# Optimization experiments

Hardware: AMD Instinct MI355X
Metric: run time of the kernel (lower is better)

Reference implementation:

```python
import jax, jax.numpy as jnp
import numpy as np

N, H, E, T = 100000, 128, 500000, 6  # nodes, hidden, max edges, edge types


def setup_inputs() -> dict:
    key = jax.random.key(0)
    ks = jax.random.split(key, 16)
    xav_e = float(np.sqrt(6.0 / (H + T * H)))  # xavier_uniform for edge_dense
    xav_h = float(np.sqrt(6.0 / (H + H)))
    u = lambda k, s, a: jax.random.uniform(k, s, jnp.float32, -a, a)
    return {
        "node_embeddings": jax.random.normal(ks[0], (N, H), jnp.float32),
        "W_edge": u(ks[1], (H, T * H), xav_e),
        "b_edge": 1e-6 * jax.random.normal(ks[2], (T * H,), jnp.float32),
        "W_ir": u(ks[3], (H, H), xav_h), "b_ir": jnp.zeros((H,), jnp.float32),
        "W_iz": u(ks[4], (H, H), xav_h), "b_iz": jnp.zeros((H,), jnp.float32),
        "W_in": u(ks[5], (H, H), xav_h), "b_in": jnp.zeros((H,), jnp.float32),
        "W_hr": u(ks[6], (H, H), xav_h),
        "W_hz": u(ks[7], (H, H), xav_h),
        "W_hn": u(ks[8], (H, H), xav_h), "b_hn": jnp.zeros((H,), jnp.float32),
        "source_indices": jax.random.randint(ks[9], (E,), 0, N, jnp.int32),
        "dest_indices": jax.random.randint(ks[10], (E,), 0, N, jnp.int32),
        "edge_types": jax.random.randint(ks[11], (E,), 0, T, jnp.int32),
        "num_edges": 450000,
    }


def reference(node_embeddings, W_edge, b_edge, W_ir, b_ir, W_iz, b_iz,
              W_in, b_in, W_hr, W_hz, W_hn, b_hn,
              source_indices, dest_indices, edge_types, num_edges):
    num_nodes, hidden = node_embeddings.shape
    max_edges = edge_types.shape[0]
    # gather source nodes, project to all edge types at once: [E, T*H]
    src = node_embeddings[source_indices]
    all_types = (src @ W_edge + b_edge).reshape(max_edges, -1, hidden)  # [E,T,H]
    # select per-edge type
    msg = jnp.take_along_axis(all_types, edge_types[:, None, None], axis=1)[:, 0, :]
    # mask padding edges, scatter-add into destination nodes
    msg = jnp.where((jnp.arange(max_edges) < num_edges)[:, None], msg, 0)
    agg = jax.ops.segment_sum(msg, dest_indices, num_segments=num_nodes)
    # GRU update: carry h = aggregated messages, inputs x = node_embeddings
    h, x = agg, node_embeddings
    r = jax.nn.sigmoid(x @ W_ir + b_ir + h @ W_hr)
    z = jax.nn.sigmoid(x @ W_iz + b_iz + h @ W_hz)
    n = jnp.tanh(x @ W_in + b_in + r * (h @ W_hn + b_hn))
    return (1.0 - z) * n + z * h
```

## Files before the change

kernel.cpp:

```cpp
#include <hip/hip_runtime.h>
#include <hip/hip_bf16.h>

#define HD 128
#define NT 6

typedef unsigned short u16;
typedef unsigned int u32;
typedef __attribute__((ext_vector_type(8))) short bf16x8;
typedef __attribute__((ext_vector_type(4))) float f32x4;

__device__ __forceinline__ float sigmoidf_(float x) {
  return 1.0f / (1.0f + __expf(-x));
}

__device__ __forceinline__ u16 f2bf(float x) {
  u32 u = __float_as_uint(x);
  return (u16)((u + 0x7FFFu + ((u >> 16) & 1u)) >> 16);
}
__device__ __forceinline__ float bflo(u32 v) { return __uint_as_float(v << 16); }
__device__ __forceinline__ float bfhi(u32 v) { return __uint_as_float(v & 0xffff0000u); }
__device__ __forceinline__ float bfs(u16 v) { return __uint_as_float((u32)v << 16); }

__device__ __forceinline__ int swz(int p) { return p ^ (((p >> 8) & 7) << 4); }

__global__ void k_cvt_w(const float* __restrict__ We,
                        const float* __restrict__ Wir, const float* __restrict__ Wiz,
                        const float* __restrict__ Win, const float* __restrict__ Whr,
                        const float* __restrict__ Whz, const float* __restrict__ Whn,
                        u16* __restrict__ WeT, u16* __restrict__ WgT) {
  int i = blockIdx.x * blockDim.x + threadIdx.x;
  if (i < NT * HD * HD) {
    int c = i >> 7, k = i & 127;
    WeT[i] = f2bf(We[(size_t)k * (NT * HD) + c]);
  } else {
    int j = i - NT * HD * HD;
    if (j < 6 * HD * HD) {
      int m = j >> 14, jj = j & 16383;
      int c = jj >> 7, k = jj & 127;
      const float* W = (m == 0) ? Wir : (m == 1) ? Wiz : (m == 2) ? Win
                     : (m == 3) ? Whr : (m == 4) ? Whz : Whn;
      WgT[j] = f2bf(W[(size_t)k * HD + c]);
    }
  }
}

__global__ __launch_bounds__(256) void k_gemm_edge6(
    const float* __restrict__ X, const u16* __restrict__ WeT,
    const float* __restrict__ Be, u16* __restrict__ P, int N)
{
  __shared__ char As[32768];
  __shared__ char Bs[32768];
  const int tid = threadIdx.x;
  const int row0 = blockIdx.x * 128;

  #pragma unroll
  for (int i = 0; i < 8; ++i) {
    int p = i * 4096 + tid * 16;
    int row = row0 + (p >> 8);
    union { u16 u[8]; bf16x8 v; } ra;
    if (row < N) {
      const float4* s = (const float4*)(X + (size_t)row0 * HD + (p >> 1));
      float4 f0 = s[0], f1 = s[1];
      ra.u[0] = f2bf(f0.x); ra.u[1] = f2bf(f0.y); ra.u[2] = f2bf(f0.z); ra.u[3] = f2bf(f0.w);
      ra.u[4] = f2bf(f1.x); ra.u[5] = f2bf(f1.y); ra.u[6] = f2bf(f1.z); ra.u[7] = f2bf(f1.w);
    } else {
      #pragma unroll
      for (int j = 0; j < 8; ++j) ra.u[j] = 0;
    }
    *(bf16x8*)(As + swz(p)) = ra.v;
  }

  const int l = tid & 63, w = tid >> 6;
  const int m0 = (w >> 1) * 64, n0 = (w & 1) * 64;
  const int lr = l & 15, lg = l >> 4;
  f32x4 zero = {0.f, 0.f, 0.f, 0.f};

  for (int t = 0; t < NT; ++t) {
    __syncthreads();
    const char* gB = (const char*)(WeT + (size_t)t * HD * HD);
    #pragma unroll
    for (int i = 0; i < 8; ++i) {
      int p = i * 4096 + tid * 16;
      *(bf16x8*)(Bs + swz(p)) = *(const bf16x8*)(gB + p);
    }
    __syncthreads();

    f32x4 acc[4][4];
    #pragma unroll
    for (int m = 0; m < 4; ++m)
      #pragma unroll
      for (int n = 0; n < 4; ++n) acc[m][n] = zero;

    #pragma unroll
    for (int k = 0; k < 4; ++k) {
      bf16x8 a[4], b[4];
      #pragma unroll
      for (int m = 0; m < 4; ++m)
        a[m] = *(const bf16x8*)(As + swz((m0 + m * 16 + lr) * 256 + k * 64 + lg * 16));
      #pragma unroll
      for (int n = 0; n < 4; ++n)
        b[n] = *(const bf16x8*)(Bs + swz((n0 + n * 16 + lr) * 256 + k * 64 + lg * 16));
      #pragma unroll
      for (int m = 0; m < 4; ++m)
        #pragma unroll
        for (int n = 0; n < 4; ++n)
          acc[m][n] = __builtin_amdgcn_mfma_f32_16x16x32_bf16(a[m], b[n], acc[m][n], 0, 0, 0);
    }

    float bias[4];
    #pragma unroll
    for (int n = 0; n < 4; ++n) bias[n] = Be[t * HD + n0 + n * 16 + lr];
    #pragma unroll
    for (int m = 0; m < 4; ++m) {
      int rbase = row0 + m0 + m * 16 + lg * 4;
      #pragma unroll
      for (int j = 0; j < 4; ++j) {
        int row = rbase + j;
        if (row < N) {
          #pragma unroll
          for (int n = 0; n < 4; ++n)
            P[(size_t)row * (NT * HD) + t * HD + n0 + n * 16 + lr] =
                f2bf(acc[m][n][j] + bias[n]);
        }
      }
    }
  }
}

__global__ __launch_bounds__(256) void k_count(const int* __restrict__ dst,
                                               const int* __restrict__ nePtr,
                                               int* __restrict__ deg) {
  const int ne = nePtr[0];
  for (int e = blockIdx.x * blockDim.x + threadIdx.x; e < ne;
       e += gridDim.x * blockDim.x)
    atomicAdd(&deg[dst[e]], 1);
}

__global__ __launch_bounds__(256) void k_scan_a(const int* __restrict__ deg,
                                                int* __restrict__ off,
                                                int* __restrict__ bsum, int N) {
  __shared__ int s[256];
  const int b = blockIdx.x, tid = threadIdx.x;
  const int base = b * 1024 + tid * 4;
  int v0 = 0, v1 = 0, v2 = 0, v3 = 0;
  if (base < N) v0 = deg[base];
  if (base + 1 < N) v1 = deg[base + 1];
  if (base + 2 < N) v2 = deg[base + 2];
  if (base + 3 < N) v3 = deg[base + 3];
  const int sum = v0 + v1 + v2 + v3;
  s[tid] = sum;
  __syncthreads();
  for (int d = 1; d < 256; d <<= 1) {
    int t = (tid >= d) ? s[tid - d] : 0;
    __syncthreads();
    s[tid] += t;
    __syncthreads();
  }
  const int excl = s[tid] - sum;
  if (base < N) off[base] = excl;
  if (base + 1 < N) off[base + 1] = excl + v0;
  if (base + 2 < N) off[base + 2] = excl + v0 + v1;
  if (base + 3 < N) off[base + 3] = excl + v0 + v1 + v2;
  if (tid == 255) bsum[b] = s[255];
}

__global__ void k_scan_b(int* __restrict__ bsum, int nb) {
  __shared__ int s[1024];
  const int tid = threadIdx.x;
  const int v = (tid < nb) ? bsum[tid] : 0;
  s[tid] = v;
  __syncthreads();
  for (int d = 1; d < 1024; d <<= 1) {
    int t = (tid >= d) ? s[tid - d] : 0;
    __syncthreads();
    s[tid] += t;
    __syncthreads();
  }
  if (tid < nb) bsum[tid] = s[tid] - v;
}

__global__ __launch_bounds__(256) void k_scan_c(int* __restrict__ off,
                                                const int* __restrict__ bsum, int N) {
  const int b = blockIdx.x, tid = threadIdx.x;
  const int add = bsum[b];
  const int base = b * 1024 + tid * 4;
  #pragma unroll
  for (int i = 0; i < 4; ++i)
    if (base + i < N) off[base + i] += add;
}

__global__ __launch_bounds__(256) void k_fill(const int* __restrict__ src,
                                              const int* __restrict__ dst,
                                              const int* __restrict__ typ,
                                              const int* __restrict__ nePtr,
                                              int* __restrict__ off,
                                              u32* __restrict__ elist) {
  const int ne = nePtr[0];
  for (int e = blockIdx.x * blockDim.x + threadIdx.x; e < ne;
       e += gridDim.x * blockDim.x) {
    int pos = atomicAdd(&off[dst[e]], 1);
    elist[pos] = (u32)(src[e] * NT + typ[e]);
  }
}

__global__ __launch_bounds__(256) void k_gather(
    const u16* __restrict__ P, const int* __restrict__ deg,
    const int* __restrict__ off, const u32* __restrict__ elist,
    u16* __restrict__ Hb, int N)
{
  const int l = threadIdx.x & 63;
  int wid = (int)((blockIdx.x * blockDim.x + threadIdx.x) >> 6);
  int nw = (int)((gridDim.x * blockDim.x) >> 6);
  for (int n = wid; n < N; n += nw) {
    const int e1 = off[n];
    const int e0 = e1 - deg[n];
    float a0 = 0.f, a1 = 0.f, b0 = 0.f, b1 = 0.f;
    for (int e = e0; e < e1; e += 4) {
      u32 p0 = elist[e];
      u32 p1 = (e + 1 < e1) ? elist[e + 1] : p0;
      u32 p2 = (e + 2 < e1) ? elist[e + 2] : p0;
      u32 p3 = (e + 3 < e1) ? elist[e + 3] : p0;
      u32 v0 = *((const u32*)(P + (size_t)p0 * HD) + l);
      u32 v1 = *((const u32*)(P + (size_t)p1 * HD) + l);
      u32 v2 = *((const u32*)(P + (size_t)p2 * HD) + l);
      u32 v3 = *((const u32*)(P + (size_t)p3 * HD) + l);
      if (e + 1 >= e1) v1 = 0;
      if (e + 2 >= e1) v2 = 0;
      if (e + 3 >= e1) v3 = 0;
      a0 += bflo(v0); a1 += bfhi(v0);
      b0 += bflo(v1); b1 += bfhi(v1);
      a0 += bflo(v2); a1 += bfhi(v2);
      b0 += bflo(v3); b1 += bfhi(v3);
    }
    a0 += b0; a1 += b1;
    u32 hp = ((u32)f2bf(a1) << 16) | (u32)f2bf(a0);
    *((u32*)(Hb + (size_t)n * HD) + l) = hp;
  }
}

__global__ __launch_bounds__(512) void k_gru15(
    const float* __restrict__ X, const u16* __restrict__ Hb,
    const u16* __restrict__ WgT,
    const float* __restrict__ bir, const float* __restrict__ biz,
    const float* __restrict__ bin_, const float* __restrict__ bhn,
    float* __restrict__ out, int N)
{
  __shared__ char Xs[32768];
  __shared__ char Hs[32768];
  __shared__ char Bs[2][32768];
  const int tid = threadIdx.x;
  const int row0 = blockIdx.x * 128;

  #pragma unroll
  for (int i = 0; i < 4; ++i) {
    int p = i * 8192 + tid * 16;
    int row = row0 + (p >> 8);
    union { u16 u[8]; bf16x8 v; } rx, rh;
    if (row < N) {
      const float4* sx = (const float4*)(X + (size_t)row0 * HD + (p >> 1));
      float4 x0 = sx[0], x1 = sx[1];
      rx.u[0] = f2bf(x0.x); rx.u[1] = f2bf(x0.y); rx.u[2] = f2bf(x0.z); rx.u[3] = f2bf(x0.w);
      rx.u[4] = f2bf(x1.x); rx.u[5] = f2bf(x1.y); rx.u[6] = f2bf(x1.z); rx.u[7] = f2bf(x1.w);
      rh.v = *(const bf16x8*)((const char*)Hb + (size_t)row0 * 256 + p);
    } else {
      #pragma unroll
      for (int j = 0; j < 8; ++j) { rx.u[j] = 0; rh.u[j] = 0; }
    }
    *(bf16x8*)(Xs + swz(p)) = rx.v;
    *(bf16x8*)(Hs + swz(p)) = rh.v;
  }

  const int l = tid & 63, w = tid >> 6;
  const int m0 = (w >> 1) * 32;
  const int n0 = (w & 1) * 64;
  const int lr = l & 15, lg = l >> 4;
  f32x4 zero = {0.f, 0.f, 0.f, 0.f};

  bf16x8 wreg[4];
  auto loadW = [&](int g) {
    const char* gp = (const char*)(WgT + (size_t)g * HD * HD);
    #pragma unroll
    for (int i = 0; i < 4; ++i)
      wreg[i] = *(const bf16x8*)(gp + i * 8192 + tid * 16);
  };
  auto writeW = [&](int buf) {
    #pragma unroll
    for (int i = 0; i < 4; ++i) {
      int p = i * 8192 + tid * 16;
      *(bf16x8*)(Bs[buf] + swz(p)) = wreg[i];
    }
  };

  auto sweep = [&](const char* Ab, int buf, f32x4 (&acc)[2][4]) {
    #pragma unroll
    for (int m = 0; m < 2; ++m)
      #pragma unroll
      for (int n = 0; n < 4; ++n) acc[m][n] = zero;
    #pragma unroll
    for (int k = 0; k < 4; ++k) {
      bf16x8 a[2], b[4];
      #pragma unroll
      for (int m = 0; m < 2; ++m)
        a[m] = *(const bf16x8*)(Ab + swz((m0 + m * 16 + lr) * 256 + k * 64 + lg * 16));
      #pragma unroll
      for (int n = 0; n < 4; ++n)
        b[n] = *(const bf16x8*)(Bs[buf] + swz((n0 + n * 16 + lr) * 256 + k * 64 + lg * 16));
      #pragma unroll
      for (int m = 0; m < 2; ++m)
        #pragma unroll
        for (int n = 0; n < 4; ++n)
          acc[m][n] = __builtin_amdgcn_mfma_f32_16x16x32_bf16(a[m], b[n], acc[m][n], 0, 0, 0);
    }
  };

  f32x4 t1[2][4], t2[2][4], rg[2][4], nn[2][4];
  float bv[4];
  auto ldBias = [&](const float* bp) {
    #pragma unroll
    for (int n = 0; n < 4; ++n) bv[n] = bp[n0 + n * 16 + lr];
  };

  loadW(0); writeW(0);
  __syncthreads();

  loadW(3);
  sweep(Xs, 0, t1);
  writeW(1);
  __syncthreads();

  loadW(5);
  sweep(Hs, 1, t2);
  writeW(0);
  ldBias(bir);
  #pragma unroll
  for (int m = 0; m < 2; ++m)
    #pragma unroll
    for (int n = 0; n < 4; ++n)
      #pragma unroll
      for (int j = 0; j < 4; ++j)
        rg[m][n][j] = sigmoidf_(t1[m][n][j] + bv[n] + t2[m][n][j]);
  __syncthreads();

  loadW(2);
  sweep(Hs, 0, t2);
  writeW(1);
  ldBias(bhn);
  #pragma unroll
  for (int m = 0; m < 2; ++m)
    #pragma unroll
    for (int n = 0; n < 4; ++n)
      #pragma unroll
      for (int j = 0; j < 4; ++j)
        rg[m][n][j] *= (t2[m][n][j] + bv[n]);
  __syncthreads();

  loadW(1);
  sweep(Xs, 1, t1);
  writeW(0);
  ldBias(bin_);
  #pragma unroll
  for (int m = 0; m < 2; ++m)
    #pragma unroll
    for (int n = 0; n < 4; ++n)
      #pragma unroll
      for (int j = 0; j < 4; ++j)
        nn[m][n][j] = tanhf(t1[m][n][j] + bv[n] + rg[m][n][j]);
  __syncthreads();

  loadW(4);
  sweep(Xs, 0, t1);
  writeW(1);
  __syncthreads();

  sweep(Hs, 1, t2);
  ldBias(biz);
  #pragma unroll
  for (int m = 0; m < 2; ++m) {
    #pragma unroll
    for (int j = 0; j < 4; ++j) {
      int row = row0 + m0 + m * 16 + lg * 4 + j;
      if (row < N) {
        #pragma unroll
        for (int n = 0; n < 4; ++n) {
          int col = n0 + n * 16 + lr;
          float z = sigmoidf_(t1[m][n][j] + bv[n] + t2[m][n][j]);
          float h = bfs(Hb[(size_t)row * HD + col]);
          out[(size_t)row * HD + col] = (1.0f - z) * nn[m][n][j] + z * h;
        }
      }
    }
  }
}

__global__ __launch_bounds__(256) void k_gather_gru(
    const float* __restrict__ X, const u16* __restrict__ P,
    const int* __restrict__ deg, const int* __restrict__ off,
    const u32* __restrict__ elist, const u16* __restrict__ WgT,
    const float* __restrict__ bir, const float* __restrict__ biz,
    const float* __restrict__ bin_, const float* __restrict__ bhn,
    float* __restrict__ out, int N)
{
  __shared__ char Xs[16384];
  __shared__ char Hs[16384];
  const int tid = threadIdx.x;
  const int l = tid & 63, w = tid >> 6;
  const int row0 = blockIdx.x * 64;
  const int wr0 = w * 16;

  #pragma unroll
  for (int it = 0; it < 4; ++it) {
    int chunk = it * 64 + l;
    int r = chunk >> 4, seg = chunk & 15;
    int grow = row0 + wr0 + r;
    union { u16 u[8]; bf16x8 v; } rx;
    if (grow < N) {
      const float4* sx = (const float4*)(X + (size_t)grow * HD + seg * 8);
      float4 x0 = sx[0], x1 = sx[1];
      rx.u[0] = f2bf(x0.x); rx.u[1] = f2bf(x0.y); rx.u[2] = f2bf(x0.z); rx.u[3] = f2bf(x0.w);
      rx.u[4] = f2bf(x1.x); rx.u[5] = f2bf(x1.y); rx.u[6] = f2bf(x1.z); rx.u[7] = f2bf(x1.w);
    } else {
      #pragma unroll
      for (int j = 0; j < 8; ++j) rx.u[j] = 0;
    }
    *(bf16x8*)(Xs + swz((wr0 + r) * 256 + seg * 16)) = rx.v;
  }

  for (int i = 0; i < 16; ++i) {
    int n = row0 + wr0 + i;
    float a0 = 0.f, a1 = 0.f;
    if (n < N) {
      int e1 = off[n];
      for (int e = e1 - deg[n]; e < e1; e += 4) {
        u32 p0 = elist[e];
        u32 p1 = (e + 1 < e1) ? elist[e + 1] : p0;
        u32 p2 = (e + 2 < e1) ? elist[e + 2] : p0;
        u32 p3 = (e + 3 < e1) ? elist[e + 3] : p0;
        u32 v0 = *((const u32*)(P + (size_t)p0 * HD) + l);
        u32 v1 = *((const u32*)(P + (size_t)p1 * HD) + l);
        u32 v2 = *((const u32*)(P + (size_t)p2 * HD) + l);
        u32 v3 = *((const u32*)(P + (size_t)p3 * HD) + l);
        if (e + 1 >= e1) v1 = 0;
        if (e + 2 >= e1) v2 = 0;
        if (e + 3 >= e1) v3 = 0;
        a0 += bflo(v0) + bflo(v1) + bflo(v2) + bflo(v3);
        a1 += bfhi(v0) + bfhi(v1) + bfhi(v2) + bfhi(v3);
      }
    }
    u32 hp = ((u32)f2bf(a1) << 16) | (u32)f2bf(a0);
    *(u32*)(Hs + swz((wr0 + i) * 256 + l * 4)) = hp;
  }

  const int lr = l & 15, lg = l >> 4;
  const int rloc = wr0;

  f32x4 zero = {0.f, 0.f, 0.f, 0.f};
  auto sweep = [&](const char* Ab, const u16* WT, f32x4* acc) {
    #pragma unroll
    for (int n = 0; n < 8; ++n) acc[n] = zero;
    #pragma unroll
    for (int k = 0; k < 4; ++k) {
      bf16x8 a = *(const bf16x8*)(Ab + swz((rloc + lr) * 256 + k * 64 + lg * 16));
      #pragma unroll
      for (int n = 0; n < 8; ++n) {
        bf16x8 b = *(const bf16x8*)(WT + (size_t)(n * 16 + lr) * HD + k * 32 + lg * 8);
        acc[n] = __builtin_amdgcn_mfma_f32_16x16x32_bf16(a, b, acc[n], 0, 0, 0);
      }
    }
  };

  f32x4 t1[8], t2[8], rg[8], nn[8];
  float bv[8];

  sweep(Xs, WgT + 0 * HD * HD, t1);
  sweep(Hs, WgT + 3 * HD * HD, t2);
  #pragma unroll
  for (int n = 0; n < 8; ++n) bv[n] = bir[n * 16 + lr];
  #pragma unroll
  for (int n = 0; n < 8; ++n)
    #pragma unroll
    for (int j = 0; j < 4; ++j) rg[n][j] = sigmoidf_(t1[n][j] + bv[n] + t2[n][j]);

  sweep(Hs, WgT + 5 * HD * HD, t2);
  #pragma unroll
  for (int n = 0; n < 8; ++n) bv[n] = bhn[n * 16 + lr];
  #pragma unroll
  for (int n = 0; n < 8; ++n)
    #pragma unroll
    for (int j = 0; j < 4; ++j) rg[n][j] *= (t2[n][j] + bv[n]);

  sweep(Xs, WgT + 2 * HD * HD, t1);
  #pragma unroll
  for (int n = 0; n < 8; ++n) bv[n] = bin_[n * 16 + lr];
  #pragma unroll
  for (int n = 0; n < 8; ++n)
    #pragma unroll
    for (int j = 0; j < 4; ++j) nn[n][j] = tanhf(t1[n][j] + bv[n] + rg[n][j]);

  sweep(Xs, WgT + 1 * HD * HD, t1);
  sweep(Hs, WgT + 4 * HD * HD, t2);
  #pragma unroll
  for (int n = 0; n < 8; ++n) bv[n] = biz[n * 16 + lr];
  #pragma unroll
  for (int n = 0; n < 8; ++n) {
    #pragma unroll
    for (int j = 0; j < 4; ++j) {
      int row = row0 + rloc + lg * 4 + j;
      if (row < N) {
        float z = sigmoidf_(t1[n][j] + bv[n] + t2[n][j]);
        u16 hu = *(const u16*)(Hs + swz((rloc + lg * 4 + j) * 256 + (n * 16 + lr) * 2));
        out[(size_t)row * HD + n * 16 + lr] = (1.0f - z) * nn[n][j] + z * bfs(hu);
      }
    }
  }
}

__global__ __launch_bounds__(256) void k_scatter(
    const u16* __restrict__ P, const int* __restrict__ src,
    const int* __restrict__ dst, const int* __restrict__ typ,
    const int* __restrict__ nePtr, float* __restrict__ agg,
    int ldP, int fixedType)
{
  const int ne = nePtr[0];
  const int lane = threadIdx.x & 63;
  const int wid = (int)((blockIdx.x * blockDim.x + threadIdx.x) >> 6);
  const int nw = (int)((gridDim.x * blockDim.x) >> 6);
  for (int e = wid; e < ne; e += nw) {
    const int t = typ[e];
    if (fixedType >= 0 && t != fixedType) continue;
    const size_t po = (ldP == HD) ? (size_t)src[e] * HD
                                  : (size_t)src[e] * (NT * HD) + (size_t)t * HD;
    u32 v = *(const u32*)(P + po + lane * 2);
    float* o = agg + (size_t)dst[e] * HD + lane * 2;
    unsafeAtomicAdd(o, bflo(v));
    unsafeAtomicAdd(o + 1, bfhi(v));
  }
}

__global__ __launch_bounds__(256) void k_gru(
    const float* __restrict__ X, const float* __restrict__ agg,
    const u16* __restrict__ WgT,
    const float* __restrict__ bir, const float* __restrict__ biz,
    const float* __restrict__ bin_, const float* __restrict__ bhn,
    float* __restrict__ out, int N)
{
  __shared__ char Xs[16384];
  __shared__ char Hs[16384];
  const int tid = threadIdx.x;
  const int row0 = blockIdx.x * 64;

  #pragma unroll
  for (int i = 0; i < 4; ++i) {
    int p = i * 4096 + tid * 16;
    int row = row0 + (p >> 8);
    union { u16 u[8]; bf16x8 v; } rx, rh;
    if (row < N) {
      const float4* sx = (const float4*)(X + (size_t)row0 * HD + (p >> 1));
      const float4* sh = (const float4*)(agg + (size_t)row0 * HD + (p >> 1));
      float4 x0 = sx[0], x1 = sx[1], h0 = sh[0], h1 = sh[1];
      rx.u[0] = f2bf(x0.x); rx.u[1] = f2bf(x0.y); rx.u[2] = f2bf(x0.z); rx.u[3] = f2bf(x0.w);
      rx.u[4] = f2bf(x1.x); rx.u[5] = f2bf(x1.y); rx.u[6] = f2bf(x1.z); rx.u[7] = f2bf(x1.w);
      rh.u[0] = f2bf(h0.x); rh.u[1] = f2bf(h0.y); rh.u[2] = f2bf(h0.z); rh.u[3] = f2bf(h0.w);
      rh.u[4] = f2bf(h1.x); rh.u[5] = f2bf(h1.y); rh.u[6] = f2bf(h1.z); rh.u[7] = f2bf(h1.w);
    } else {
      #pragma unroll
      for (int j = 0; j < 8; ++j) { rx.u[j] = 0; rh.u[j] = 0; }
    }
    *(bf16x8*)(Xs + swz(p)) = rx.v;
    *(bf16x8*)(Hs + swz(p)) = rh.v;
  }
  __syncthreads();

  const int l = tid & 63, w = tid >> 6;
  const int lr = l & 15, lg = l >> 4;
  const int rloc = w * 16;

  f32x4 zero = {0.f, 0.f, 0.f, 0.f};
  auto sweep = [&](const char* Ab, const u16* WT, f32x4* acc) {
    #pragma unroll
    for (int n = 0; n < 8; ++n) acc[n] = zero;
    #pragma unroll
    for (int k = 0; k < 4; ++k) {
      bf16x8 a = *(const bf16x8*)(Ab + swz((rloc + lr) * 256 + k * 64 + lg * 16));
      #pragma unroll
      for (int n = 0; n < 8; ++n) {
        bf16x8 b = *(const bf16x8*)(WT + (size_t)(n * 16 + lr) * HD + k * 32 + lg * 8);
        acc[n] = __builtin_amdgcn_mfma_f32_16x16x32_bf16(a, b, acc[n], 0, 0, 0);
      }
    }
  };

  f32x4 t1[8], t2[8], rg[8], nn[8];
  float bv[8];

  sweep(Xs, WgT + 0 * HD * HD, t1);
  sweep(Hs, WgT + 3 * HD * HD, t2);
  #pragma unroll
  for (int n = 0; n < 8; ++n) bv[n] = bir[n * 16 + lr];
  #pragma unroll
  for (int n = 0; n < 8; ++n)
    #pragma unroll
    for (int j = 0; j < 4; ++j) rg[n][j] = sigmoidf_(t1[n][j] + bv[n] + t2[n][j]);

  sweep(Hs, WgT + 5 * HD * HD, t2);
  #pragma unroll
  for (int n = 0; n < 8; ++n) bv[n] = bhn[n * 16 + lr];
  #pragma unroll
  for (int n = 0; n < 8; ++n)
    #pragma unroll
    for (int j = 0; j < 4; ++j) rg[n][j] *= (t2[n][j] + bv[n]);

  sweep(Xs, WgT + 2 * HD * HD, t1);
  #pragma unroll
  for (int n = 0; n < 8; ++n) bv[n] = bin_[n * 16 + lr];
  #pragma unroll
  for (int n = 0; n < 8; ++n)
    #pragma unroll
    for (int j = 0; j < 4; ++j) nn[n][j] = tanhf(t1[n][j] + bv[n] + rg[n][j]);

  sweep(Xs, WgT + 1 * HD * HD, t1);
  sweep(Hs, WgT + 4 * HD * HD, t2);
  #pragma unroll
  for (int n = 0; n < 8; ++n) bv[n] = biz[n * 16 + lr];
  #pragma unroll
  for (int n = 0; n < 8; ++n) {
    #pragma unroll
    for (int j = 0; j < 4; ++j) {
      int row = row0 + rloc + lg * 4 + j;
      if (row < N) {
        float z = sigmoidf_(t1[n][j] + bv[n] + t2[n][j]);
        float h = agg[(size_t)row * HD + n * 16 + lr];
        out[(size_t)row * HD + n * 16 + lr] = (1.0f - z) * nn[n][j] + z * h;
      }
    }
  }
}

extern "C" void kernel_launch(void* const* d_in, const int* in_sizes, int n_in,
                              void* d_out, int out_size, void* d_ws, size_t ws_size,
                              hipStream_t stream) {
  const float* X      = (const float*)d_in[0];
  const float* W_edge = (const float*)d_in[1];
  const float* b_edge = (const float*)d_in[2];
  const float* b_ir   = (const float*)d_in[4];
  const float* b_iz   = (const float*)d_in[6];
  const float* b_in   = (const float*)d_in[8];
  const float* b_hn   = (const float*)d_in[12];
  const int* src      = (const int*)d_in[13];
  const int* dst      = (const int*)d_in[14];
  const int* typ      = (const int*)d_in[15];
  const int* nePtr    = (const int*)d_in[16];

  const int N = in_sizes[0] / HD;
  const int E = in_sizes[13];
  char* ws = (char*)d_ws;

  size_t cur = 0;
  auto alloc = [&](size_t bytes) {
    size_t p = cur;
    cur = (cur + bytes + 255) & ~(size_t)255;
    return p;
  };
  u16* WeT   = (u16*)(ws + alloc((size_t)NT * HD * HD * 2));
  u16* WgT   = (u16*)(ws + alloc((size_t)6 * HD * HD * 2));
  int* deg   = (int*)(ws + alloc((size_t)N * 4));
  int* offA  = (int*)(ws + alloc((size_t)N * 4));
  int* bsum  = (int*)(ws + alloc(1024 * 4));
  u32* elist = (u32*)(ws + alloc((size_t)E * 4));
  size_t base_need = cur;
  u16* P     = (u16*)(ws + alloc((size_t)N * NT * HD * 2));
  const size_t csr_need = cur;
  u16* Hb    = (u16*)(ws + alloc((size_t)N * HD * 2));
  const size_t split_need = cur;

  const int gb = (N + 127) / 128;
  const int NB = (N + 1023) / 1024;

  k_cvt_w<<<(NT * HD * HD + 6 * HD * HD + 255) / 256, 256, 0, stream>>>(
      W_edge, (const float*)d_in[3], (const float*)d_in[5], (const float*)d_in[7],
      (const float*)d_in[9], (const float*)d_in[10], (const float*)d_in[11], WeT, WgT);

  if (ws_size >= csr_need) {
    hipMemsetAsync(deg, 0, (size_t)N * 4, stream);
    k_gemm_edge6<<<gb, 256, 0, stream>>>(X, WeT, b_edge, P, N);
    k_count<<<1024, 256, 0, stream>>>(dst, nePtr, deg);
    k_scan_a<<<NB, 256, 0, stream>>>(deg, offA, bsum, N);
    k_scan_b<<<1, 1024, 0, stream>>>(bsum, NB);
    k_scan_c<<<NB, 256, 0, stream>>>(offA, bsum, N);
    k_fill<<<1024, 256, 0, stream>>>(src, dst, typ, nePtr, offA, elist);
    if (ws_size >= split_need) {
      k_gather<<<(N + 3) / 4, 256, 0, stream>>>(P, deg, offA, elist, Hb, N);
      k_gru15<<<gb, 512, 0, stream>>>(
          X, Hb, WgT, b_ir, b_iz, b_in, b_hn, (float*)d_out, N);
    } else {
      k_gather_gru<<<(N + 63) / 64, 256, 0, stream>>>(
          X, P, deg, offA, elist, WgT, b_ir, b_iz, b_in, b_hn, (float*)d_out, N);
    }
  } else {
    float* agg = (float*)d_out;
    hipMemsetAsync(d_out, 0, (size_t)out_size * sizeof(float), stream);
    size_t pneed = base_need + (size_t)N * NT * HD * 2;
    if (ws_size >= pneed) {
      u16* Pf = (u16*)(ws + base_need);
      k_gemm_edge6<<<gb, 256, 0, stream>>>(X, WeT, b_edge, Pf, N);
      k_scatter<<<2048, 256, 0, stream>>>(Pf, src, dst, typ, nePtr, agg, NT * HD, -1);
      k_gru<<<(N + 63) / 64, 256, 0, stream>>>(X, agg, WgT, b_ir, b_iz, b_in, b_hn, agg, N);
    }
  }
}
```

Baseline: 236.6 us.

## Fuse CSR gather into LDS-staged GRU kernel, drop separate gather pass

Replaces the separate gather kernel and split GRU kernel with one fused kernel. Each 512-thread block gathers the aggregated messages for its 128 rows straight into shared memory, then runs the double-buffered LDS weight GEMM pipeline. The bf16 Hb intermediate no longer makes a global round trip and one launch goes away. The cost is that the irregular gather now shares occupancy with a 128KB-LDS block, so gather latency hiding may suffer.

```diff
diff --git a/kernel.cpp b/kernel.cpp
--- a/kernel.cpp
+++ b/kernel.cpp
@@ -203,44 +203,10 @@
   }
 }
 
-__global__ __launch_bounds__(256) void k_gather(
-    const u16* __restrict__ P, const int* __restrict__ deg,
-    const int* __restrict__ off, const u32* __restrict__ elist,
-    u16* __restrict__ Hb, int N)
-{
-  const int l = threadIdx.x & 63;
-  int wid = (int)((blockIdx.x * blockDim.x + threadIdx.x) >> 6);
-  int nw = (int)((gridDim.x * blockDim.x) >> 6);
-  for (int n = wid; n < N; n += nw) {
-    const int e1 = off[n];
-    const int e0 = e1 - deg[n];
-    float a0 = 0.f, a1 = 0.f, b0 = 0.f, b1 = 0.f;
-    for (int e = e0; e < e1; e += 4) {
-      u32 p0 = elist[e];
-      u32 p1 = (e + 1 < e1) ? elist[e + 1] : p0;
-      u32 p2 = (e + 2 < e1) ? elist[e + 2] : p0;
-      u32 p3 = (e + 3 < e1) ? elist[e + 3] : p0;
-      u32 v0 = *((const u32*)(P + (size_t)p0 * HD) + l);
-      u32 v1 = *((const u32*)(P + (size_t)p1 * HD) + l);
-      u32 v2 = *((const u32*)(P + (size_t)p2 * HD) + l);
-      u32 v3 = *((const u32*)(P + (size_t)p3 * HD) + l);
-      if (e + 1 >= e1) v1 = 0;
-      if (e + 2 >= e1) v2 = 0;
-      if (e + 3 >= e1) v3 = 0;
-      a0 += bflo(v0); a1 += bfhi(v0);
-      b0 += bflo(v1); b1 += bfhi(v1);
-      a0 += bflo(v2); a1 += bfhi(v2);
-      b0 += bflo(v3); b1 += bfhi(v3);
-    }
-    a0 += b0; a1 += b1;
-    u32 hp = ((u32)f2bf(a1) << 16) | (u32)f2bf(a0);
-    *((u32*)(Hb + (size_t)n * HD) + l) = hp;
-  }
-}
-
-__global__ __launch_bounds__(512) void k_gru15(
-    const float* __restrict__ X, const u16* __restrict__ Hb,
-    const u16* __restrict__ WgT,
+__global__ __launch_bounds__(512) void k_gru16(
+    const float* __restrict__ X, const u16* __restrict__ P,
+    const int* __restrict__ deg, const int* __restrict__ off,
+    const u32* __restrict__ elist, const u16* __restrict__ WgT,
     const float* __restrict__ bir, const float* __restrict__ biz,
     const float* __restrict__ bin_, const float* __restrict__ bhn,
     float* __restrict__ out, int N)
@@ -249,32 +215,9 @@
   __shared__ char Hs[32768];
   __shared__ char Bs[2][32768];
   const int tid = threadIdx.x;
+  const int l = tid & 63, w = tid >> 6;
   const int row0 = blockIdx.x * 128;
-
-  #pragma unroll
-  for (int i = 0; i < 4; ++i) {
-    int p = i * 8192 + tid * 16;
-    int row = row0 + (p >> 8);
-    union { u16 u[8]; bf16x8 v; } rx, rh;
-    if (row < N) {
-      const float4* sx = (const float4*)(X + (size_t)row0 * HD + (p >> 1));
-      float4 x0 = sx[0], x1 = sx[1];
-      rx.u[0] = f2bf(x0.x); rx.u[1] = f2bf(x0.y); rx.u[2] = f2bf(x0.z); rx.u[3] = f2bf(x0.w);
-      rx.u[4] = f2bf(x1.x); rx.u[5] = f2bf(x1.y); rx.u[6] = f2bf(x1.z); rx.u[7] = f2bf(x1.w);
-      rh.v = *(const bf16x8*)((const char*)Hb + (size_t)row0 * 256 + p);
-    } else {
-      #pragma unroll
-      for (int j = 0; j < 8; ++j) { rx.u[j] = 0; rh.u[j] = 0; }
-    }
-    *(bf16x8*)(Xs + swz(p)) = rx.v;
-    *(bf16x8*)(Hs + swz(p)) = rh.v;
-  }
-
-  const int l = tid & 63, w = tid >> 6;
-  const int m0 = (w >> 1) * 32;
-  const int n0 = (w & 1) * 64;
-  const int lr = l & 15, lg = l >> 4;
-  f32x4 zero = {0.f, 0.f, 0.f, 0.f};
+  const int wr0 = w * 16;
 
   bf16x8 wreg[4];
   auto loadW = [&](int g) {
@@ -291,121 +234,7 @@
     }
   };
 
-  auto sweep = [&](const char* Ab, int buf, f32x4 (&acc)[2][4]) {
-    #pragma unroll
-    for (int m = 0; m < 2; ++m)
-      #pragma unroll
-      for (int n = 0; n < 4; ++n) acc[m][n] = zero;
-    #pragma unroll
-    for (int k = 0; k < 4; ++k) {
-      bf16x8 a[2], b[4];
-      #pragma unroll
-      for (int m = 0; m < 2; ++m)
-        a[m] = *(const bf16x8*)(Ab + swz((m0 + m * 16 + lr) * 256 + k * 64 + lg * 16));
-      #pragma unroll
-      for (int n = 0; n < 4; ++n)
-        b[n] = *(const bf16x8*)(Bs[buf] + swz((n0 + n * 16 + lr) * 256 + k * 64 + lg * 16));
-      #pragma unroll
-      for (int m = 0; m < 2; ++m)
-        #pragma unroll
-        for (int n = 0; n < 4; ++n)
-          acc[m][n] = __builtin_amdgcn_mfma_f32_16x16x32_bf16(a[m], b[n], acc[m][n], 0, 0, 0);
-    }
-  };
-
-  f32x4 t1[2][4], t2[2][4], rg[2][4], nn[2][4];
-  float bv[4];
-  auto ldBias = [&](const float* bp) {
-    #pragma unroll
-    for (int n = 0; n < 4; ++n) bv[n] = bp[n0 + n * 16 + lr];
-  };
-
-  loadW(0); writeW(0);
-  __syncthreads();
-
-  loadW(3);
-  sweep(Xs, 0, t1);
-  writeW(1);
-  __syncthreads();
-
-  loadW(5);
-  sweep(Hs, 1, t2);
-  writeW(0);
-  ldBias(bir);
-  #pragma unroll
-  for (int m = 0; m < 2; ++m)
-    #pragma unroll
-    for (int n = 0; n < 4; ++n)
-      #pragma unroll
-      for (int j = 0; j < 4; ++j)
-        rg[m][n][j] = sigmoidf_(t1[m][n][j] + bv[n] + t2[m][n][j]);
-  __syncthreads();
-
-  loadW(2);
-  sweep(Hs, 0, t2);
-  writeW(1);
-  ldBias(bhn);
-  #pragma unroll
-  for (int m = 0; m < 2; ++m)
-    #pragma unroll
-    for (int n = 0; n < 4; ++n)
-      #pragma unroll
-      for (int j = 0; j < 4; ++j)
-        rg[m][n][j] *= (t2[m][n][j] + bv[n]);
-  __syncthreads();
-
-  loadW(1);
-  sweep(Xs, 1, t1);
-  writeW(0);
-  ldBias(bin_);
-  #pragma unroll
-  for (int m = 0; m < 2; ++m)
-    #pragma unroll
-    for (int n = 0; n < 4; ++n)
-      #pragma unroll
-      for (int j = 0; j < 4; ++j)
-        nn[m][n][j] = tanhf(t1[m][n][j] + bv[n] + rg[m][n][j]);
-  __syncthreads();
-
-  loadW(4);
-  sweep(Xs, 0, t1);
-  writeW(1);
-  __syncthreads();
-
-  sweep(Hs, 1, t2);
-  ldBias(biz);
-  #pragma unroll
-  for (int m = 0; m < 2; ++m) {
-    #pragma unroll
-    for (int j = 0; j < 4; ++j) {
-      int row = row0 + m0 + m * 16 + lg * 4 + j;
-      if (row < N) {
-        #pragma unroll
-        for (int n = 0; n < 4; ++n) {
-          int col = n0 + n * 16 + lr;
-          float z = sigmoidf_(t1[m][n][j] + bv[n] + t2[m][n][j]);
-          float h = bfs(Hb[(size_t)row * HD + col]);
-          out[(size_t)row * HD + col] = (1.0f - z) * nn[m][n][j] + z * h;
-        }
-      }
-    }
-  }
-}
-
-__global__ __launch_bounds__(256) void k_gather_gru(
-    const float* __restrict__ X, const u16* __restrict__ P,
-    const int* __restrict__ deg, const int* __restrict__ off,
-    const u32* __restrict__ elist, const u16* __restrict__ WgT,
-    const float* __restrict__ bir, const float* __restrict__ biz,
-    const float* __restrict__ bin_, const float* __restrict__ bhn,
-    float* __restrict__ out, int N)
-{
-  __shared__ char Xs[16384];
-  __shared__ char Hs[16384];
-  const int tid = threadIdx.x;
-  const int l = tid & 63, w = tid >> 6;
-  const int row0 = blockIdx.x * 64;
-  const int wr0 = w * 16;
+  loadW(0);
 
   #pragma unroll
   for (int it = 0; it < 4; ++it) {
@@ -427,7 +256,7 @@
 
   for (int i = 0; i < 16; ++i) {
     int n = row0 + wr0 + i;
-    float a0 = 0.f, a1 = 0.f;
+    float a0 = 0.f, a1 = 0.f, b0 = 0.f, b1 = 0.f;
     if (n < N) {
       int e1 = off[n];
       for (int e = e1 - deg[n]; e < e1; e += 4) {
@@ -442,73 +271,119 @@
         if (e + 1 >= e1) v1 = 0;
         if (e + 2 >= e1) v2 = 0;
         if (e + 3 >= e1) v3 = 0;
-        a0 += bflo(v0) + bflo(v1) + bflo(v2) + bflo(v3);
-        a1 += bfhi(v0) + bfhi(v1) + bfhi(v2) + bfhi(v3);
+        a0 += bflo(v0); a1 += bfhi(v0);
+        b0 += bflo(v1); b1 += bfhi(v1);
+        a0 += bflo(v2); a1 += bfhi(v2);
+        b0 += bflo(v3); b1 += bfhi(v3);
       }
     }
+    a0 += b0; a1 += b1;
     u32 hp = ((u32)f2bf(a1) << 16) | (u32)f2bf(a0);
     *(u32*)(Hs + swz((wr0 + i) * 256 + l * 4)) = hp;
   }
 
+  const int m0 = (w >> 1) * 32;
+  const int n0 = (w & 1) * 64;
   const int lr = l & 15, lg = l >> 4;
-  const int rloc = wr0;
-
   f32x4 zero = {0.f, 0.f, 0.f, 0.f};
-  auto sweep = [&](const char* Ab, const u16* WT, f32x4* acc) {
-    #pragma unroll
-    for (int n = 0; n < 8; ++n) acc[n] = zero;
+
+  auto sweep = [&](const char* Ab, int buf, f32x4 (&acc)[2][4]) {
+    #pragma unroll
+    for (int m = 0; m < 2; ++m)
+      #pragma unroll
+      for (int n = 0; n < 4; ++n) acc[m][n] = zero;
     #pragma unroll
     for (int k = 0; k < 4; ++k) {
-      bf16x8 a = *(const bf16x8*)(Ab + swz((rloc + lr) * 256 + k * 64 + lg * 16));
-      #pragma unroll
-      for (int n = 0; n < 8; ++n) {
-        bf16x8 b = *(const bf16x8*)(WT + (size_t)(n * 16 + lr) * HD + k * 32 + lg * 8);
-        acc[n] = __builtin_amdgcn_mfma_f32_16x16x32_bf16(a, b, acc[n], 0, 0, 0);
-      }
+      bf16x8 a[2], b[4];
+      #pragma unroll
+      for (int m = 0; m < 2; ++m)
+        a[m] = *(const bf16x8*)(Ab + swz((m0 + m * 16 + lr) * 256 + k * 64 + lg * 16));
+      #pragma unroll
+      for (int n = 0; n < 4; ++n)
+        b[n] = *(const bf16x8*)(Bs[buf] + swz((n0 + n * 16 + lr) * 256 + k * 64 + lg * 16));
+      #pragma unroll
+      for (int m = 0; m < 2; ++m)
+        #pragma unroll
+        for (int n = 0; n < 4; ++n)
+          acc[m][n] = __builtin_amdgcn_mfma_f32_16x16x32_bf16(a[m], b[n], acc[m][n], 0, 0, 0);
     }
   };
 
-  f32x4 t1[8], t2[8], rg[8], nn[8];
-  float bv[8];
-
-  sweep(Xs, WgT + 0 * HD * HD, t1);
-  sweep(Hs, WgT + 3 * HD * HD, t2);
-  #pragma unroll
-  for (int n = 0; n < 8; ++n) bv[n] = bir[n * 16 + lr];
-  #pragma unroll
-  for (int n = 0; n < 8; ++n)
-    #pragma unroll
-    for (int j = 0; j < 4; ++j) rg[n][j] = sigmoidf_(t1[n][j] + bv[n] + t2[n][j]);
-
-  sweep(Hs, WgT + 5 * HD * HD, t2);
-  #pragma unroll
-  for (int n = 0; n < 8; ++n) bv[n] = bhn[n * 16 + lr];
-  #pragma unroll
-  for (int n = 0; n < 8; ++n)
-    #pragma unroll
-    for (int j = 0; j < 4; ++j) rg[n][j] *= (t2[n][j] + bv[n]);
-
-  sweep(Xs, WgT + 2 * HD * HD, t1);
-  #pragma unroll
-  for (int n = 0; n < 8; ++n) bv[n] = bin_[n * 16 + lr];
-  #pragma unroll
-  for (int n = 0; n < 8; ++n)
-    #pragma unroll
-    for (int j = 0; j < 4; ++j) nn[n][j] = tanhf(t1[n][j] + bv[n] + rg[n][j]);
-
-  sweep(Xs, WgT + 1 * HD * HD, t1);
-  sweep(Hs, WgT + 4 * HD * HD, t2);
-  #pragma unroll
-  for (int n = 0; n < 8; ++n) bv[n] = biz[n * 16 + lr];
-  #pragma unroll
-  for (int n = 0; n < 8; ++n) {
+  f32x4 t1[2][4], t2[2][4], rg[2][4], nn[2][4];
+  float bv[4];
+  auto ldBias = [&](const float* bp) {
+    #pragma unroll
+    for (int n = 0; n < 4; ++n) bv[n] = bp[n0 + n * 16 + lr];
+  };
+
+  writeW(0);
+  __syncthreads();
+
+  loadW(3);
+  sweep(Xs, 0, t1);
+  writeW(1);
+  __syncthreads();
+
+  loadW(5);
+  sweep(Hs, 1, t2);
+  writeW(0);
+  ldBias(bir);
+  #pragma unroll
+  for (int m = 0; m < 2; ++m)
+    #pragma unroll
+    for (int n = 0; n < 4; ++n)
+      #pragma unroll
+      for (int j = 0; j < 4; ++j)
+        rg[m][n][j] = sigmoidf_(t1[m][n][j] + bv[n] + t2[m][n][j]);
+  __syncthreads();
+
+  loadW(2);
+  sweep(Hs, 0, t2);
+  writeW(1);
+  ldBias(bhn);
+  #pragma unroll
+  for (int m = 0; m < 2; ++m)
+    #pragma unroll
+    for (int n = 0; n < 4; ++n)
+      #pragma unroll
+      for (int j = 0; j < 4; ++j)
+        rg[m][n][j] *= (t2[m][n][j] + bv[n]);
+  __syncthreads();
+
+  loadW(1);
+  sweep(Xs, 1, t1);
+  writeW(0);
+  ldBias(bin_);
+  #pragma unroll
+  for (int m = 0; m < 2; ++m)
+    #pragma unroll
+    for (int n = 0; n < 4; ++n)
+      #pragma unroll
+      for (int j = 0; j < 4; ++j)
+        nn[m][n][j] = tanhf(t1[m][n][j] + bv[n] + rg[m][n][j]);
+  __syncthreads();
+
+  loadW(4);
+  sweep(Xs, 0, t1);
+  writeW(1);
+  __syncthreads();
+
+  sweep(Hs, 1, t2);
+  ldBias(biz);
+  #pragma unroll
+  for (int m = 0; m < 2; ++m) {
     #pragma unroll
     for (int j = 0; j < 4; ++j) {
-      int row = row0 + rloc + lg * 4 + j;
+      int rloc = m0 + m * 16 + lg * 4 + j;
+      int row = row0 + rloc;
       if (row < N) {
-        float z = sigmoidf_(t1[n][j] + bv[n] + t2[n][j]);
-        u16 hu = *(const u16*)(Hs + swz((rloc + lg * 4 + j) * 256 + (n * 16 + lr) * 2));
-        out[(size_t)row * HD + n * 16 + lr] = (1.0f - z) * nn[n][j] + z * bfs(hu);
+        #pragma unroll
+        for (int n = 0; n < 4; ++n) {
+          int col = n0 + n * 16 + lr;
+          float z = sigmoidf_(t1[m][n][j] + bv[n] + t2[m][n][j]);
+          u16 hu = *(const u16*)(Hs + swz(rloc * 256 + col * 2));
+          out[(size_t)row * HD + col] = (1.0f - z) * nn[m][n][j] + z * bfs(hu);
+        }
       }
     }
   }
@@ -669,8 +544,6 @@
   size_t base_need = cur;
   u16* P     = (u16*)(ws + alloc((size_t)N * NT * HD * 2));
   const size_t csr_need = cur;
-  u16* Hb    = (u16*)(ws + alloc((size_t)N * HD * 2));
-  const size_t split_need = cur;
 
   const int gb = (N + 127) / 128;
   const int NB = (N + 1023) / 1024;
@@ -687,14 +560,8 @@
     k_scan_b<<<1, 1024, 0, stream>>>(bsum, NB);
     k_scan_c<<<NB, 256, 0, stream>>>(offA, bsum, N);
     k_fill<<<1024, 256, 0, stream>>>(src, dst, typ, nePtr, offA, elist);
-    if (ws_size >= split_need) {
-      k_gather<<<(N + 3) / 4, 256, 0, stream>>>(P, deg, offA, elist, Hb, N);
-      k_gru15<<<gb, 512, 0, stream>>>(
-          X, Hb, WgT, b_ir, b_iz, b_in, b_hn, (float*)d_out, N);
-    } else {
-      k_gather_gru<<<(N + 63) / 64, 256, 0, stream>>>(
-          X, P, deg, offA, elist, WgT, b_ir, b_iz, b_in, b_hn, (float*)d_out, N);
-    }
+    k_gru16<<<gb, 512, 0, stream>>>(
+        X, P, deg, offA, elist, WgT, b_ir, b_iz, b_in, b_hn, (float*)d_out, N);
   } else {
     float* agg = (float*)d_out;
     hipMemsetAsync(d_out, 0, (size_t)out_size * sizeof(float), stream);
```

Measured after the change: 297.8 us. 1.26x slower.
